# Kernel tuning notes

Hardware: AMD Instinct MI355X
Metric: run time of the kernel (lower is better)

## Reference

```python
import jax, jax.numpy as jnp
import numpy as np

B, F, H, E, C, K = 32768, 1024, 512, 10, 10, 4  # batch, in_features, hidden, f_enc, num_classes, n_branches


def setup_inputs() -> dict:
    key = jax.random.key(0)
    ks = jax.random.split(key, 12)
    def rn(k, shape, scale):
        return jax.random.normal(k, shape, jnp.float32) * scale
    return {
        "w0": rn(ks[0], (B, F), 1.0),
        "w1": rn(ks[1], (B, F), 1.0),
        "w2": rn(ks[2], (B, F), 1.0),
        "w3": rn(ks[3], (B, F), 1.0),
        # 4 branch linears in -> hidden, stacked on leading axis
        "Wlin": rn(ks[4], (K, H, F), F ** -0.5),
        "blin": jnp.zeros((K, H), jnp.float32),
        # per-branch Q/K/V projections hidden -> f_enc
        "Wq": rn(ks[5], (K, E, H), H ** -0.5),
        "bq": jnp.zeros((K, E), jnp.float32),
        "Wk": rn(ks[6], (K, E, H), H ** -0.5),
        "bk": jnp.zeros((K, E), jnp.float32),
        "Wv": rn(ks[7], (K, E, H), H ** -0.5),
        "bv": jnp.zeros((K, E), jnp.float32),
        # 4 final classifier heads f_enc -> num_classes
        "Wfin": rn(ks[8], (K, C, E), E ** -0.5),
        "bfin": jnp.zeros((K, C), jnp.float32),
    }


def reference(w0, w1, w2, w3, Wlin, blin, Wq, bq, Wk, bk, Wv, bv, Wfin, bfin):
    # dropout is identity in eval mode
    w = jnp.stack([w0, w1, w2, w3], axis=1)              # [B,K,F]
    h = jnp.einsum('bkf,khf->bkh', w, Wlin) + blin        # [B,K,H]
    q = jnp.einsum('bkh,keh->bke', h, Wq) + bq            # [B,K,E]
    k_enc = jnp.einsum('bkh,keh->bke', h, Wk) + bk        # [B,K,E]
    v = jnp.einsum('bkh,keh->bke', h, Wv) + bv            # [B,K,E]
    # einsum 'bij,bil->bjl' contracts the branch axis (i == K)
    attn = jnp.einsum('bke,bkl->bel', q, k_enc) / np.float32(np.sqrt(E))  # [B,E,E]
    attn = jax.nn.softmax(attn, axis=1)                   # torch Softmax(dim=1)
    att_out = jnp.einsum('bnm,bkm->bkn', attn, v)         # [B,K,E]
    w0o = att_out[:, 0, :]                                # original uses index 0 for all four heads
    logits = jnp.einsum('be,kce->bkc', w0o, Wfin) + bfin  # [B,K,C]
    outputs = jnp.mean(jax.nn.softmax(logits, axis=-1), axis=1)  # 0.25 * sum of 4 softmaxed heads
    return (outputs, attn)
```

## Files before the change

### kernel.cpp

```cpp
#include <hip/hip_runtime.h>
#include <stdint.h>

#define B_ROWS 32768
#define F_DIM  1024
#define H_DIM  512
#define RS     32832

typedef __attribute__((ext_vector_type(4))) float    floatx4;
typedef __attribute__((ext_vector_type(2))) __fp16   fp16x2;
typedef __attribute__((ext_vector_type(8))) _Float16 halfx8;

__device__ __forceinline__ void async_load16(const void* g, void* l) {
    __builtin_amdgcn_global_load_lds(
        (const __attribute__((address_space(1))) void*)g,
        (__attribute__((address_space(3))) void*)l, 16, 0, 0);
}

__global__ __launch_bounds__(128) void k_prep(
    const float* __restrict__ Wlin, const float* __restrict__ blin,
    const float* __restrict__ Wq, const float* __restrict__ Wk,
    const float* __restrict__ Wv, const float* __restrict__ bq,
    const float* __restrict__ bk, const float* __restrict__ bv,
    ushort* __restrict__ Wcomb16, float* __restrict__ bcomb)
{
    const int bx   = blockIdx.x;
    const int k    = bx >> 6;
    const int d    = (bx >> 1) & 31;
    const int half = bx & 1;
    const int t    = threadIdx.x;
    const int col  = half * 512 + t * 4;
    ushort4* outp = (ushort4*)(Wcomb16 + ((size_t)(k * 32 + d) << 10) + col);

    if (d >= 30) {
        ushort4 z; z.x = z.y = z.z = z.w = 0;
        *outp = z;
        if (half == 0 && t == 0) bcomb[k * 32 + d] = 0.f;
        return;
    }

    const float* wrow; float bias;
    if (d < 10)      { wrow = Wq + (size_t)(k * 10 + d) * H_DIM;      bias = bq[k * 10 + d]; }
    else if (d < 20) { wrow = Wk + (size_t)(k * 10 + d - 10) * H_DIM; bias = bk[k * 10 + d - 10]; }
    else             { wrow = Wv + (size_t)(k * 10 + d - 20) * H_DIM; bias = bv[k * 10 + d - 20]; }

    const float* wl = Wlin + ((size_t)k * H_DIM << 10) + col;
    const float* bl = blin + (size_t)k * H_DIM;

    floatx4 acc = {0.f, 0.f, 0.f, 0.f};
    float bacc = 0.f;
    #pragma unroll 8
    for (int h = 0; h < H_DIM; ++h) {
        const float s = wrow[h];
        const floatx4 x = *(const floatx4*)(wl + ((size_t)h << 10));
        acc.x += s * x.x; acc.y += s * x.y; acc.z += s * x.z; acc.w += s * x.w;
        bacc += s * bl[h];
    }
    union { _Float16 h[4]; ushort4 u; } o;
    o.h[0] = (_Float16)acc.x; o.h[1] = (_Float16)acc.y;
    o.h[2] = (_Float16)acc.z; o.h[3] = (_Float16)acc.w;
    *outp = o.u;
    if (half == 0 && t == 0) bcomb[k * 32 + d] = bias + bacc;
}

__global__ __launch_bounds__(256) void k_main(
    const float* __restrict__ w0, const float* __restrict__ w1,
    const float* __restrict__ w2, const float* __restrict__ w3,
    const ushort* __restrict__ Wcomb16, const float* __restrict__ bcomb,
    float* __restrict__ qkv_t)
{
    __shared__ float  As[2][128 * 64];
    __shared__ ushort Bs[2][32 * 64];

    const int tid     = threadIdx.x;
    const int bx      = blockIdx.x;
    const int k       = bx & 3;
    const int rowBase = (bx >> 2) * 128;

    const float* A = (k == 0) ? w0 : (k == 1) ? w1 : (k == 2) ? w2 : w3;

    const int arow  = tid >> 4;
    const int ascol = ((tid & 15) ^ (arow & 7)) * 4;
    const int brow  = tid >> 3;
    const int bscol = ((tid & 7) ^ (brow & 7)) * 8;

    const float*  gA0 = A + (size_t)(rowBase + arow) * F_DIM + ascol;
    const ushort* gB0 = Wcomb16 + (size_t)(k * 32 + brow) * 1024 + bscol;

    const int wv = tid >> 6;
    const int ln = tid & 63;
    const int lr = ln & 15;
    const int lq = ln >> 4;
    const int sw = lr & 7;

    floatx4 acc[2][2] = {};

    #define STAGE(buf, kc) do {                                            \
        float*  lAb = &As[buf][tid * 4];                                   \
        ushort* lBb = &Bs[buf][tid * 8];                                   \
        _Pragma("unroll")                                                  \
        for (int it = 0; it < 8; ++it)                                     \
            async_load16(gA0 + (kc) + it * 16 * F_DIM, lAb + it * 16 * 64);\
        async_load16(gB0 + (kc), lBb);                                     \
    } while (0)

    STAGE(0, 0);

    #pragma unroll 2
    for (int t = 0; t < 16; ++t) {
        const int cur = t & 1;
        if (t < 15) {
            STAGE(cur ^ 1, (t + 1) * 64);
            asm volatile("s_waitcnt vmcnt(9)" ::: "memory");
        } else {
            asm volatile("s_waitcnt vmcnt(0)" ::: "memory");
        }
        __builtin_amdgcn_sched_barrier(0);
        __builtin_amdgcn_s_barrier();
        __builtin_amdgcn_sched_barrier(0);

        #pragma unroll
        for (int ks = 0; ks < 2; ++ks) {
            halfx8 af[2];
            #pragma unroll
            for (int i = 0; i < 2; ++i) {
                const int rbase = (wv * 32 + i * 16 + lr) * 64;
                const int s0 = (ks * 8 + lq * 2) ^ sw;
                const floatx4 f0 = *(const floatx4*)&As[cur][rbase + s0 * 4];
                const floatx4 f1 = *(const floatx4*)&As[cur][rbase + (s0 ^ 1) * 4];
                union { fp16x2 h2[4]; halfx8 h8; } u;
                u.h2[0] = __builtin_amdgcn_cvt_pkrtz(f0.x, f0.y);
                u.h2[1] = __builtin_amdgcn_cvt_pkrtz(f0.z, f0.w);
                u.h2[2] = __builtin_amdgcn_cvt_pkrtz(f1.x, f1.y);
                u.h2[3] = __builtin_amdgcn_cvt_pkrtz(f1.z, f1.w);
                af[i] = u.h8;
            }
            #pragma unroll
            for (int j = 0; j < 2; ++j) {
                const int bs = (ks * 4 + lq) ^ sw;
                const halfx8 bf = *(const halfx8*)&Bs[cur][(j * 16 + lr) * 64 + bs * 8];
                acc[0][j] = __builtin_amdgcn_mfma_f32_16x16x32_f16(af[0], bf, acc[0][j], 0, 0, 0);
                acc[1][j] = __builtin_amdgcn_mfma_f32_16x16x32_f16(af[1], bf, acc[1][j], 0, 0, 0);
            }
        }
        __builtin_amdgcn_sched_barrier(0);
        __builtin_amdgcn_s_barrier();
    }
    #undef STAGE

    const float* bc = bcomb + k * 32;
    #pragma unroll
    for (int j = 0; j < 2; ++j) {
        const int d = j * 16 + lr;
        if (d < 30) {
            const float bias = bc[d];
            float* outd = qkv_t + (size_t)(k * 30 + d) * RS;
            #pragma unroll
            for (int i = 0; i < 2; ++i) {
                const int r0 = rowBase + wv * 32 + i * 16 + lq * 4;
                floatx4 o = acc[i][j];
                o.x += bias; o.y += bias; o.z += bias; o.w += bias;
                *(floatx4*)(outd + r0) = o;
            }
        }
    }
}

__global__ __launch_bounds__(128) void k_final(
    const float* __restrict__ qkv_t, const float* __restrict__ Wfin,
    const float* __restrict__ bfin,
    float* __restrict__ outputs, float* __restrict__ attn)
{
    __shared__ float sW[400];
    __shared__ float sb[40];
    __shared__ float sA[128 * 101];
    const int t = threadIdx.x;
    for (int i = t; i < 400; i += 128) sW[i] = Wfin[i];
    if (t < 40) sb[t] = bfin[t];
    __syncthreads();

    const int b = blockIdx.x * 128 + t;
    const float* pt = qkv_t + b;
    float q[4][10], kk[4][10], v0[10];
    #pragma unroll
    for (int k = 0; k < 4; ++k)
        #pragma unroll
        for (int e = 0; e < 10; ++e) {
            q[k][e]  = pt[(size_t)(k * 30 + e) * RS];
            kk[k][e] = pt[(size_t)(k * 30 + 10 + e) * RS];
        }
    #pragma unroll
    for (int m = 0; m < 10; ++m) v0[m] = pt[(size_t)(20 + m) * RS];

    float out0[10];
    #pragma unroll
    for (int e = 0; e < 10; ++e) out0[e] = 0.f;
    float* sAr = &sA[t * 101];
    const float inv = 0.31622776601683794f;

    #pragma unroll
    for (int m = 0; m < 10; ++m) {
        float col[10]; float mx = -1e30f;
        #pragma unroll
        for (int e = 0; e < 10; ++e) {
            col[e] = (q[0][e]*kk[0][m] + q[1][e]*kk[1][m]
                    + q[2][e]*kk[2][m] + q[3][e]*kk[3][m]) * inv;
            mx = fmaxf(mx, col[e]);
        }
        float s = 0.f;
        #pragma unroll
        for (int e = 0; e < 10; ++e) { col[e] = __expf(col[e] - mx); s += col[e]; }
        const float r = 1.f / s;
        #pragma unroll
        for (int e = 0; e < 10; ++e) {
            const float a = col[e] * r;
            sAr[e * 10 + m] = a;
            out0[e] += a * v0[m];
        }
    }

    float oc[10];
    #pragma unroll
    for (int c = 0; c < 10; ++c) oc[c] = 0.f;
    #pragma unroll
    for (int k = 0; k < 4; ++k) {
        float lg[10]; float mx = -1e30f;
        #pragma unroll
        for (int c = 0; c < 10; ++c) {
            float s = sb[k * 10 + c];
            #pragma unroll
            for (int e = 0; e < 10; ++e) s += out0[e] * sW[(k * 10 + c) * 10 + e];
            lg[c] = s; mx = fmaxf(mx, s);
        }
        float s = 0.f;
        #pragma unroll
        for (int c = 0; c < 10; ++c) { lg[c] = __expf(lg[c] - mx); s += lg[c]; }
        const float r = 0.25f / s;
        #pragma unroll
        for (int c = 0; c < 10; ++c) oc[c] += lg[c] * r;
    }

    __syncthreads();
    const size_t abase = (size_t)blockIdx.x * 12800;
    for (int i = t; i < 12800; i += 128) {
        const int bl = i / 100;
        attn[abase + i] = sA[bl * 101 + (i - bl * 100)];
    }

    __syncthreads();
    #pragma unroll
    for (int c = 0; c < 10; ++c) sA[t * 11 + c] = oc[c];
    __syncthreads();
    const size_t obase = (size_t)blockIdx.x * 1280;
    for (int i = t; i < 1280; i += 128) {
        const int bl = i / 10;
        outputs[obase + i] = sA[bl * 11 + (i - bl * 10)];
    }
}

extern "C" void kernel_launch(void* const* d_in, const int* in_sizes, int n_in,
                              void* d_out, int out_size, void* d_ws, size_t ws_size,
                              hipStream_t stream) {
    const float* w0   = (const float*)d_in[0];
    const float* w1   = (const float*)d_in[1];
    const float* w2   = (const float*)d_in[2];
    const float* w3   = (const float*)d_in[3];
    const float* Wlin = (const float*)d_in[4];
    const float* blin = (const float*)d_in[5];
    const float* Wq   = (const float*)d_in[6];
    const float* bq   = (const float*)d_in[7];
    const float* Wk   = (const float*)d_in[8];
    const float* bk   = (const float*)d_in[9];
    const float* Wv   = (const float*)d_in[10];
    const float* bv   = (const float*)d_in[11];
    const float* Wfin = (const float*)d_in[12];
    const float* bfin = (const float*)d_in[13];

    char* ws = (char*)d_ws;
    ushort* Wcomb16 = (ushort*)ws;
    float*  bcomb   = (float*)(ws + ((size_t)256 << 10));
    float*  qkv_t   = (float*)(ws + ((size_t)1 << 20));

    float* outputs = (float*)d_out;
    float* attn    = outputs + (size_t)B_ROWS * 10;

    k_prep <<<256,  128, 0, stream>>>(Wlin, blin, Wq, Wk, Wv, bq, bk, bv, Wcomb16, bcomb);
    k_main <<<1024, 256, 0, stream>>>(w0, w1, w2, w3, Wcomb16, bcomb, qkv_t);
    k_final<<<256,  128, 0, stream>>>(qkv_t, Wfin, bfin, outputs, attn);
}
```

Baseline: 518.4 us.

## Stage full weight tile in LDS and stream A directly into registers

The main GEMM kernel now loads the whole fp16 combined weight slice into LDS once per block. The fp32 input rows are read straight from global memory into registers with a two-deep software prefetch, which removes the per-iteration LDS staging and barriers for A. Blocks grow to 512 threads covering 256 rows. V projections for branches other than 0 are no longer stored, since only branch 0's values are used. The prep kernel caches the weight row and bias in shared memory and splits its accumulation. The trade-offs are less coalesced global access patterns for A and larger LDS use per block, which may limit occupancy.

```diff
diff --git a/kernel.cpp b/kernel.cpp
--- a/kernel.cpp
+++ b/kernel.cpp
@@ -16,25 +16,27 @@
         (__attribute__((address_space(3))) void*)l, 16, 0, 0);
 }
 
-__global__ __launch_bounds__(128) void k_prep(
+__global__ __launch_bounds__(64) void k_prep(
     const float* __restrict__ Wlin, const float* __restrict__ blin,
     const float* __restrict__ Wq, const float* __restrict__ Wk,
     const float* __restrict__ Wv, const float* __restrict__ bq,
     const float* __restrict__ bk, const float* __restrict__ bv,
     ushort* __restrict__ Wcomb16, float* __restrict__ bcomb)
 {
-    const int bx   = blockIdx.x;
-    const int k    = bx >> 6;
-    const int d    = (bx >> 1) & 31;
-    const int half = bx & 1;
-    const int t    = threadIdx.x;
-    const int col  = half * 512 + t * 4;
-    ushort4* outp = (ushort4*)(Wcomb16 + ((size_t)(k * 32 + d) << 10) + col);
+    __shared__ float sw_[H_DIM];
+    __shared__ float sbl[H_DIM];
+    const int bx = blockIdx.x;
+    const int k  = bx >> 7;
+    const int d  = (bx >> 2) & 31;
+    const int qd = bx & 3;
+    const int t  = threadIdx.x;
+    const int col = qd * 256 + t * 4;
+    ushort4* outp = (ushort4*)(Wcomb16 + (((size_t)(k * 32 + d)) << 10) + col);
 
     if (d >= 30) {
         ushort4 z; z.x = z.y = z.z = z.w = 0;
         *outp = z;
-        if (half == 0 && t == 0) bcomb[k * 32 + d] = 0.f;
+        if (qd == 0 && t == 0) bcomb[k * 32 + d] = 0.f;
         return;
     }
 
@@ -43,48 +45,56 @@
     else if (d < 20) { wrow = Wk + (size_t)(k * 10 + d - 10) * H_DIM; bias = bk[k * 10 + d - 10]; }
     else             { wrow = Wv + (size_t)(k * 10 + d - 20) * H_DIM; bias = bv[k * 10 + d - 20]; }
 
-    const float* wl = Wlin + ((size_t)k * H_DIM << 10) + col;
     const float* bl = blin + (size_t)k * H_DIM;
-
-    floatx4 acc = {0.f, 0.f, 0.f, 0.f};
-    float bacc = 0.f;
+    for (int i = t; i < H_DIM; i += 64) { sw_[i] = wrow[i]; sbl[i] = bl[i]; }
+    __syncthreads();
+
+    const float* wl = Wlin + (((size_t)k * H_DIM) << 10) + col;
+
+    floatx4 acc0 = {0.f,0.f,0.f,0.f}, acc1 = {0.f,0.f,0.f,0.f};
+    float ba0 = 0.f, ba1 = 0.f;
     #pragma unroll 8
-    for (int h = 0; h < H_DIM; ++h) {
-        const float s = wrow[h];
-        const floatx4 x = *(const floatx4*)(wl + ((size_t)h << 10));
-        acc.x += s * x.x; acc.y += s * x.y; acc.z += s * x.z; acc.w += s * x.w;
-        bacc += s * bl[h];
-    }
+    for (int h = 0; h < H_DIM; h += 2) {
+        const float s0 = sw_[h], s1 = sw_[h + 1];
+        const floatx4 x0 = *(const floatx4*)(wl + ((size_t)h << 10));
+        const floatx4 x1 = *(const floatx4*)(wl + ((size_t)(h + 1) << 10));
+        acc0 += x0 * s0;
+        acc1 += x1 * s1;
+        ba0 += s0 * sbl[h];
+        ba1 += s1 * sbl[h + 1];
+    }
+    const floatx4 acc = acc0 + acc1;
     union { _Float16 h[4]; ushort4 u; } o;
     o.h[0] = (_Float16)acc.x; o.h[1] = (_Float16)acc.y;
     o.h[2] = (_Float16)acc.z; o.h[3] = (_Float16)acc.w;
     *outp = o.u;
-    if (half == 0 && t == 0) bcomb[k * 32 + d] = bias + bacc;
-}
-
-__global__ __launch_bounds__(256) void k_main(
+    if (qd == 0 && t == 0) bcomb[k * 32 + d] = bias + ba0 + ba1;
+}
+
+__global__ __launch_bounds__(512, 4) void k_main(
     const float* __restrict__ w0, const float* __restrict__ w1,
     const float* __restrict__ w2, const float* __restrict__ w3,
     const ushort* __restrict__ Wcomb16, const float* __restrict__ bcomb,
     float* __restrict__ qkv_t)
 {
-    __shared__ float  As[2][128 * 64];
-    __shared__ ushort Bs[2][32 * 64];
+    __shared__ ushort Bs[32 * 1024];
 
     const int tid     = threadIdx.x;
     const int bx      = blockIdx.x;
     const int k       = bx & 3;
-    const int rowBase = (bx >> 2) * 128;
+    const int rowBase = (bx >> 2) * 256;
 
     const float* A = (k == 0) ? w0 : (k == 1) ? w1 : (k == 2) ? w2 : w3;
 
-    const int arow  = tid >> 4;
-    const int ascol = ((tid & 15) ^ (arow & 7)) * 4;
-    const int brow  = tid >> 3;
-    const int bscol = ((tid & 7) ^ (brow & 7)) * 8;
-
-    const float*  gA0 = A + (size_t)(rowBase + arow) * F_DIM + ascol;
-    const ushort* gB0 = Wcomb16 + (size_t)(k * 32 + brow) * 1024 + bscol;
+    #pragma unroll
+    for (int it = 0; it < 8; ++it) {
+        const int s   = it * 512 + tid;
+        const int row = s >> 7;
+        const int g   = (s & 127) ^ (row & 7);
+        async_load16(Wcomb16 + (((size_t)(k * 32 + row)) << 10) + g * 8,
+                     (ushort*)Bs + (size_t)s * 8);
+    }
+    __syncthreads();
 
     const int wv = tid >> 6;
     const int ln = tid & 63;
@@ -92,66 +102,55 @@
     const int lq = ln >> 4;
     const int sw = lr & 7;
 
+    const float* aP0 = A + (size_t)(rowBase + wv * 32 + lr) * F_DIM + lq * 8;
+    const float* aP1 = aP0 + (size_t)16 * F_DIM;
+
     floatx4 acc[2][2] = {};
 
-    #define STAGE(buf, kc) do {                                            \
-        float*  lAb = &As[buf][tid * 4];                                   \
-        ushort* lBb = &Bs[buf][tid * 8];                                   \
-        _Pragma("unroll")                                                  \
-        for (int it = 0; it < 8; ++it)                                     \
-            async_load16(gA0 + (kc) + it * 16 * F_DIM, lAb + it * 16 * 64);\
-        async_load16(gB0 + (kc), lBb);                                     \
-    } while (0)
-
-    STAGE(0, 0);
-
+#define LOADC(kc, b0, b1, b2, b3) do {                       \
+    b0 = *(const floatx4*)(aP0 + (kc));                      \
+    b1 = *(const floatx4*)(aP0 + (kc) + 4);                  \
+    b2 = *(const floatx4*)(aP1 + (kc));                      \
+    b3 = *(const floatx4*)(aP1 + (kc) + 4);                  \
+} while (0)
+
+#define COMPUTE(t, b0, b1, b2, b3) do {                                      \
+    union { fp16x2 h2[4]; halfx8 h8; } u0, u1;                               \
+    u0.h2[0] = __builtin_amdgcn_cvt_pkrtz(b0.x, b0.y);                       \
+    u0.h2[1] = __builtin_amdgcn_cvt_pkrtz(b0.z, b0.w);                       \
+    u0.h2[2] = __builtin_amdgcn_cvt_pkrtz(b1.x, b1.y);                       \
+    u0.h2[3] = __builtin_amdgcn_cvt_pkrtz(b1.z, b1.w);                       \
+    u1.h2[0] = __builtin_amdgcn_cvt_pkrtz(b2.x, b2.y);                       \
+    u1.h2[1] = __builtin_amdgcn_cvt_pkrtz(b2.z, b2.w);                       \
+    u1.h2[2] = __builtin_amdgcn_cvt_pkrtz(b3.x, b3.y);                       \
+    u1.h2[3] = __builtin_amdgcn_cvt_pkrtz(b3.z, b3.w);                       \
+    const int slot_ = (((t) * 4 + lq) ^ sw) * 8;                             \
+    const halfx8 bf0 = *(const halfx8*)&Bs[(lr << 10) + slot_];              \
+    const halfx8 bf1 = *(const halfx8*)&Bs[((16 + lr) << 10) + slot_];       \
+    acc[0][0] = __builtin_amdgcn_mfma_f32_16x16x32_f16(u0.h8, bf0, acc[0][0], 0, 0, 0); \
+    acc[0][1] = __builtin_amdgcn_mfma_f32_16x16x32_f16(u0.h8, bf1, acc[0][1], 0, 0, 0); \
+    acc[1][0] = __builtin_amdgcn_mfma_f32_16x16x32_f16(u1.h8, bf0, acc[1][0], 0, 0, 0); \
+    acc[1][1] = __builtin_amdgcn_mfma_f32_16x16x32_f16(u1.h8, bf1, acc[1][1], 0, 0, 0); \
+} while (0)
+
+    floatx4 a0, a1, a2, a3, c0, c1, c2, c3;
+    LOADC(0, a0, a1, a2, a3);
     #pragma unroll 2
-    for (int t = 0; t < 16; ++t) {
-        const int cur = t & 1;
-        if (t < 15) {
-            STAGE(cur ^ 1, (t + 1) * 64);
-            asm volatile("s_waitcnt vmcnt(9)" ::: "memory");
-        } else {
-            asm volatile("s_waitcnt vmcnt(0)" ::: "memory");
-        }
-        __builtin_amdgcn_sched_barrier(0);
-        __builtin_amdgcn_s_barrier();
-        __builtin_amdgcn_sched_barrier(0);
-
-        #pragma unroll
-        for (int ks = 0; ks < 2; ++ks) {
-            halfx8 af[2];
-            #pragma unroll
-            for (int i = 0; i < 2; ++i) {
-                const int rbase = (wv * 32 + i * 16 + lr) * 64;
-                const int s0 = (ks * 8 + lq * 2) ^ sw;
-                const floatx4 f0 = *(const floatx4*)&As[cur][rbase + s0 * 4];
-                const floatx4 f1 = *(const floatx4*)&As[cur][rbase + (s0 ^ 1) * 4];
-                union { fp16x2 h2[4]; halfx8 h8; } u;
-                u.h2[0] = __builtin_amdgcn_cvt_pkrtz(f0.x, f0.y);
-                u.h2[1] = __builtin_amdgcn_cvt_pkrtz(f0.z, f0.w);
-                u.h2[2] = __builtin_amdgcn_cvt_pkrtz(f1.x, f1.y);
-                u.h2[3] = __builtin_amdgcn_cvt_pkrtz(f1.z, f1.w);
-                af[i] = u.h8;
-            }
-            #pragma unroll
-            for (int j = 0; j < 2; ++j) {
-                const int bs = (ks * 4 + lq) ^ sw;
-                const halfx8 bf = *(const halfx8*)&Bs[cur][(j * 16 + lr) * 64 + bs * 8];
-                acc[0][j] = __builtin_amdgcn_mfma_f32_16x16x32_f16(af[0], bf, acc[0][j], 0, 0, 0);
-                acc[1][j] = __builtin_amdgcn_mfma_f32_16x16x32_f16(af[1], bf, acc[1][j], 0, 0, 0);
-            }
-        }
-        __builtin_amdgcn_sched_barrier(0);
-        __builtin_amdgcn_s_barrier();
-    }
-    #undef STAGE
-
-    const float* bc = bcomb + k * 32;
+    for (int t = 0; t < 32; t += 2) {
+        LOADC((t + 1) * 32, c0, c1, c2, c3);
+        COMPUTE(t, a0, a1, a2, a3);
+        if (t + 2 < 32) LOADC((t + 2) * 32, a0, a1, a2, a3);
+        COMPUTE(t + 1, c0, c1, c2, c3);
+    }
+#undef LOADC
+#undef COMPUTE
+
+    const float* bc   = bcomb + k * 32;
+    const int    dmax = (k == 0) ? 30 : 20;
     #pragma unroll
     for (int j = 0; j < 2; ++j) {
         const int d = j * 16 + lr;
-        if (d < 30) {
+        if (d < dmax) {
             const float bias = bc[d];
             float* outd = qkv_t + (size_t)(k * 30 + d) * RS;
             #pragma unroll
@@ -283,7 +282,7 @@
     float* outputs = (float*)d_out;
     float* attn    = outputs + (size_t)B_ROWS * 10;
 
-    k_prep <<<256,  128, 0, stream>>>(Wlin, blin, Wq, Wk, Wv, bq, bk, bv, Wcomb16, bcomb);
-    k_main <<<1024, 256, 0, stream>>>(w0, w1, w2, w3, Wcomb16, bcomb, qkv_t);
-    k_final<<<256,  128, 0, stream>>>(qkv_t, Wfin, bfin, outputs, attn);
-}
+    k_prep <<<512, 64,  0, stream>>>(Wlin, blin, Wq, Wk, Wv, bq, bk, bv, Wcomb16, bcomb);
+    k_main <<<512, 512, 0, stream>>>(w0, w1, w2, w3, Wcomb16, bcomb, qkv_t);
+    k_final<<<256, 128, 0, stream>>>(qkv_t, Wfin, bfin, outputs, attn);
+}
```

After: 583.1 us. 1.12x slower.
